# Kernel optimization log

Hardware: AMD Instinct MI355X
Metric: run time of the kernel (lower is better)

Reference implementation:

```python
import jax, jax.numpy as jnp
import numpy as np

H, KVH, HD = 32, 8, 128
DM = 4096
LN_L, LN_R = 64, 64
K_BITS, V_BITS = 4, 4
ROPE_THETA = 10000.0


def _rope(x, pos):
    # x: [B, nH, S, D], pos: [B, S]
    D = x.shape[-1]
    inv_freq = 1.0 / (ROPE_THETA ** (jnp.arange(0, D, 2, dtype=jnp.float32) / D))
    freqs = pos[:, :, None].astype(jnp.float32) * inv_freq            # [B,S,D/2]
    emb = jnp.concatenate([freqs, freqs], axis=-1)                     # [B,S,D]
    cos = jnp.cos(emb)[:, None, :, :]
    sin = jnp.sin(emb)[:, None, :, :]
    x1, x2 = x[..., : D // 2], x[..., D // 2:]
    rot = jnp.concatenate([-x2, x1], axis=-1)
    return x * cos + rot * sin


def _fake_quant(x, bits):
    # per-token (last-dim row) symmetric fake quantization
    qmax = 2.0 ** (bits - 1) - 1.0
    s = jnp.maximum(jnp.max(jnp.abs(x), axis=-1, keepdims=True) / qmax, 1e-8)
    return jnp.clip(jnp.round(x / s), -qmax, qmax) * s


def setup_inputs() -> dict:
    key = jax.random.key(0)
    ks = jax.random.split(key, 10)
    B, S = 1, 2048
    hidden_states = jax.random.normal(ks[0], (B, S, DM), dtype=jnp.float32)
    causal = jnp.tril(jnp.ones((S, S), dtype=bool))
    attention_mask = jnp.where(causal, 0.0, -1e9).astype(jnp.float32)[None, None]  # [1,1,S,S]
    position_ids = jnp.arange(S, dtype=jnp.int32)[None, :]
    sc = 1.0 / np.sqrt(DM)
    Wq = jax.random.normal(ks[1], (DM, H * HD), dtype=jnp.float32) * sc
    Wk = jax.random.normal(ks[2], (DM, KVH * HD), dtype=jnp.float32) * sc
    Wv = jax.random.normal(ks[3], (DM, KVH * HD), dtype=jnp.float32) * sc
    Wo = jax.random.normal(ks[4], (H * HD, DM), dtype=jnp.float32) * (1.0 / np.sqrt(H * HD))
    ln_left = jnp.eye(LN_L, dtype=jnp.float32) + 0.02 * jax.random.normal(ks[5], (LN_L, LN_L), dtype=jnp.float32)
    ln_right = jnp.eye(LN_R, dtype=jnp.float32) + 0.02 * jax.random.normal(ks[6], (LN_R, LN_R), dtype=jnp.float32)
    Tk = jnp.eye(HD, dtype=jnp.float32) + 0.05 * jax.random.normal(ks[7], (HD, HD), dtype=jnp.float32)
    Tv = jnp.eye(HD, dtype=jnp.float32) + 0.05 * jax.random.normal(ks[8], (HD, HD), dtype=jnp.float32)
    return {"hidden_states": hidden_states, "attention_mask": attention_mask,
            "position_ids": position_ids, "ln_left": ln_left, "ln_right": ln_right,
            "Wq": Wq, "Wk": Wk, "Wv": Wv, "Wo": Wo, "Tk": Tk, "Tv": Tv}


def reference(hidden_states, attention_mask, position_ids,
              ln_left, ln_right, Wq, Wk, Wv, Wo, Tk, Tv):
    B, S, _ = hidden_states.shape
    # ln_trans: Kronecker-decomposed SVD transform on hidden dim (64x64)
    h = hidden_states.reshape(B, S, LN_L, LN_R)
    h = jnp.einsum('bslr,la,rc->bsac', h, ln_left, ln_right).reshape(B, S, DM)
    # q/k/v projections (effective, trans-absorbed weights)
    q = (h @ Wq).reshape(B, S, H, HD).transpose(0, 2, 1, 3)    # [B,H,S,hd]
    k = (h @ Wk).reshape(B, S, KVH, HD).transpose(0, 2, 1, 3)  # [B,KVH,S,hd]
    v = ((h @ Wv).reshape(B, S, KVH, HD) @ Tv).transpose(0, 2, 1, 3)  # vcache_trans on V
    # RoPE
    q = _rope(q, position_ids)
    k = _rope(k, position_ids)
    # kcache_trans: q gets inv-transpose, k gets forward transform, then fake-quant K
    Tk_inv_t = jnp.linalg.inv(Tk).T
    q = q @ Tk_inv_t
    k = _fake_quant(k @ Tk, K_BITS)
    # vcache quant
    v = _fake_quant(v, V_BITS)
    # GQA repeat
    rep = H // KVH
    k = jnp.repeat(k, rep, axis=1)
    v = jnp.repeat(v, rep, axis=1)
    scores = jnp.einsum('bhqd,bhkd->bhqk', q, k) / np.sqrt(HD) + attention_mask
    p = jax.nn.softmax(scores.astype(jnp.float32), axis=-1).astype(q.dtype)
    o = jnp.einsum('bhqk,bhkd->bhqd', p, v).transpose(0, 2, 1, 3)  # [B,S,H,hd]
    # undo vcache_trans per head, then output projection
    o = o @ jnp.linalg.inv(Tv)
    return o.reshape(B, S, DM) @ Wo
```

## Files before the change

### kernel.cpp

```cpp
#include <hip/hip_runtime.h>
#include <math.h>

#define S_    2048
#define DM_   4096
#define H_    32
#define KVH_  8
#define HD_   128

typedef __bf16 bf16x8 __attribute__((ext_vector_type(8)));
typedef float  f32x4  __attribute__((ext_vector_type(4)));
typedef unsigned short u16x8 __attribute__((ext_vector_type(8)));
typedef unsigned short ushort_t;

__device__ __forceinline__ ushort_t f2b(float f) {
  unsigned int u = __float_as_uint(f);
  unsigned int r = (u + 0x7fffu + ((u >> 16) & 1u)) >> 16;
  return (ushort_t)r;
}
__device__ __forceinline__ float b2f(ushort_t h) {
  return __uint_as_float(((unsigned int)h) << 16);
}
__device__ __forceinline__ bf16x8 asbf(u16x8 v) {
  return __builtin_bit_cast(bf16x8, v);
}

__device__ __forceinline__ void gload16(const void* g, void* l) {
  __builtin_amdgcn_global_load_lds(
      (const __attribute__((address_space(1))) void*)g,
      (__attribute__((address_space(3))) void*)(unsigned int)(unsigned long long)l,
      16, 0, 0);
}

__global__ void newton_init(const float* __restrict__ A0, const float* __restrict__ A1,
                            float* __restrict__ X0, float* __restrict__ X1)
{
  const float* A = blockIdx.x ? A1 : A0;
  float*       X = blockIdx.x ? X1 : X0;
  const int i = blockIdx.y * 1024 + threadIdx.x;
  const int r = i >> 7, c = i & 127;
  X[i] = ((r == c) ? 2.0f : 0.0f) - A[i];
}

__global__ __launch_bounds__(256) void nmm(
    const float* __restrict__ A0, const float* __restrict__ B0, float* __restrict__ C0, int tr0,
    const float* __restrict__ A1, const float* __restrict__ B1, float* __restrict__ C1, int tr1,
    int update)
{
  const float* A = blockIdx.y ? A1 : A0;
  const float* B = blockIdx.y ? B1 : B0;
  float*       C = blockIdx.y ? C1 : C0;
  const int tr   = blockIdx.y ? tr1 : tr0;
  const int m0   = blockIdx.x * 32;
  const int tid  = threadIdx.x;

  __shared__ float Bs[128][132];
  __shared__ float As[32][132];

#pragma unroll
  for (int i = 0; i < 16; ++i) {
    int idx = tid + i * 256;
    int row = idx >> 5, c4 = (idx & 31) * 4;
    *(float4*)&Bs[row][c4] = *(const float4*)&B[row * 128 + c4];
  }
#pragma unroll
  for (int i = 0; i < 4; ++i) {
    int idx = tid + i * 256;
    int row = idx >> 5, c4 = (idx & 31) * 4;
    *(float4*)&As[row][c4] = *(const float4*)&A[(m0 + row) * 128 + c4];
  }
  __syncthreads();

  const int rloc = tid >> 3;
  const int c0   = (tid & 7) * 16;
  float acc[16];
#pragma unroll
  for (int j = 0; j < 16; ++j) acc[j] = 0.0f;
  for (int k = 0; k < 128; ++k) {
    float a = As[rloc][k];
#pragma unroll
    for (int j = 0; j < 16; j += 4) {
      float4 bv = *(const float4*)&Bs[k][c0 + j];
      acc[j + 0] += a * bv.x; acc[j + 1] += a * bv.y;
      acc[j + 2] += a * bv.z; acc[j + 3] += a * bv.w;
    }
  }
#pragma unroll
  for (int j = 0; j < 16; ++j) {
    float v = update ? (2.0f * As[rloc][c0 + j] - acc[j]) : acc[j];
    if (tr) C[(c0 + j) * 128 + (m0 + rloc)] = v;
    else    C[(m0 + rloc) * 128 + c0 + j]   = v;
  }
}

__global__ void ttrans(const float* __restrict__ in, float* __restrict__ out)
{
  __shared__ float t[32][33];
  const int bx = blockIdx.x * 32, by = blockIdx.y * 32;
  const int r = threadIdx.x >> 5, c = threadIdx.x & 31;
#pragma unroll
  for (int i = 0; i < 4; ++i)
    t[r + i * 8][c] = in[(by + r + i * 8) * 128 + bx + c];
  __syncthreads();
#pragma unroll
  for (int i = 0; i < 4; ++i)
    out[(bx + r + i * 8) * 128 + by + c] = t[c][r + i * 8];
}

__global__ void tfrag_prep(const float* __restrict__ T0, const float* __restrict__ T1,
                           const float* __restrict__ T2,
                           ushort_t* __restrict__ Fhi, ushort_t* __restrict__ Flo)
{
  const int mat = blockIdx.x;
  const float* src = (mat == 0) ? T0 : ((mat == 1) ? T1 : T2);
  ushort_t* hi = Fhi + mat * 16384;
  ushort_t* lo = Flo + mat * 16384;
  const int t = threadIdx.x;
  for (int ch = 0; ch < 32; ++ch) {
    int nt = ch >> 2, ds = ch & 3;
#pragma unroll
    for (int i = 0; i < 2; ++i) {
      int idx = t + i * 256;
      int ln = idx >> 3, j = idx & 7;
      int cc = ln & 15, gg = ln >> 4;
      int d = ds * 32 + gg * 8 + j, n = nt * 16 + cc;
      float x = src[d * 128 + n];
      ushort_t hb = f2b(x);
      hi[(ch << 9) + idx] = hb;
      lo[(ch << 9) + idx] = f2b(x - b2f(hb));
    }
  }
}

__global__ void rope_table(const int* __restrict__ pos,
                           float* __restrict__ cosT, float* __restrict__ sinT)
{
  const int s = blockIdx.x, i = threadIdx.x;
  float invf = 1.0f / (float)pow(10000.0, (double)i * (1.0 / 64.0));
  float ang  = (float)pos[s] * invf;
  cosT[s * 64 + i] = cosf(ang);
  sinT[s * 64 + i] = sinf(ang);
}

__global__ __launch_bounds__(256) void ln2(const float* __restrict__ hid,
                                           const float* __restrict__ L,
                                           const float* __restrict__ R,
                                           ushort_t* __restrict__ hb16,
                                           ushort_t* __restrict__ hlo16)
{
  __shared__ float B0[64 * 68];
  __shared__ float B1[64 * 68];
  __shared__ float B2[64 * 68];
  const int s   = blockIdx.x;
  const int tid = threadIdx.x;
  const float* hrow = hid + (size_t)s * DM_;

  for (int i = tid; i < 1024; i += 256) {
    int rr = i >> 4, q4 = (i & 15) * 4;
    *(float4*)&B0[rr * 68 + q4] = *(const float4*)&hrow[rr * 64 + q4];
    *(float4*)&B1[rr * 68 + q4] = *(const float4*)&R[rr * 64 + q4];
  }
  __syncthreads();

  const int row = tid >> 2;
  const int c0  = (tid & 3) * 16;
  float acc[16];
#pragma unroll
  for (int j = 0; j < 16; ++j) acc[j] = 0.0f;
  for (int rr = 0; rr < 64; ++rr) {
    float hv = B0[row * 68 + rr];
#pragma unroll
    for (int j = 0; j < 16; j += 4) {
      float4 rv = *(const float4*)&B1[rr * 68 + c0 + j];
      acc[j + 0] += hv * rv.x; acc[j + 1] += hv * rv.y;
      acc[j + 2] += hv * rv.z; acc[j + 3] += hv * rv.w;
    }
  }
#pragma unroll
  for (int j = 0; j < 16; j += 4)
    *(float4*)&B2[row * 68 + c0 + j] = make_float4(acc[j], acc[j+1], acc[j+2], acc[j+3]);
  __syncthreads();
  for (int i = tid; i < 1024; i += 256) {
    int rr = i >> 4, q4 = (i & 15) * 4;
    *(float4*)&B1[rr * 68 + q4] = *(const float4*)&L[rr * 64 + q4];
  }
  __syncthreads();

#pragma unroll
  for (int j = 0; j < 16; ++j) acc[j] = 0.0f;
  for (int ll = 0; ll < 64; ++ll) {
    float lv = B1[ll * 68 + row];
#pragma unroll
    for (int j = 0; j < 16; j += 4) {
      float4 tv = *(const float4*)&B2[ll * 68 + c0 + j];
      acc[j + 0] += lv * tv.x; acc[j + 1] += lv * tv.y;
      acc[j + 2] += lv * tv.z; acc[j + 3] += lv * tv.w;
    }
  }
  const size_t base = (size_t)s * DM_ + row * 64 + c0;
  u16x8 hv0, hv1, lv0, lv1;
#pragma unroll
  for (int j = 0; j < 8; ++j) {
    ushort_t h = f2b(acc[j]);     hv0[j] = h; lv0[j] = f2b(acc[j] - b2f(h));
    ushort_t g = f2b(acc[j + 8]); hv1[j] = g; lv1[j] = f2b(acc[j + 8] - b2f(g));
  }
  *(u16x8*)&hb16[base]      = hv0;
  *(u16x8*)&hb16[base + 8]  = hv1;
  *(u16x8*)&hlo16[base]     = lv0;
  *(u16x8*)&hlo16[base + 8] = lv1;
}

__global__ void wtrans(const float* __restrict__ W, ushort_t* __restrict__ WT,
                       int K, int N)
{
  __shared__ ushort_t t[64][68];
  const int tid = threadIdx.x;
  const int n0 = blockIdx.x * 64, k0 = blockIdx.y * 64;
  for (int idx = tid; idx < 4096; idx += 256) {
    int rr = idx >> 6, cc = idx & 63;
    t[cc][rr] = f2b(W[(size_t)(k0 + rr) * N + n0 + cc]);
  }
  __syncthreads();
  for (int idx = tid; idx < 4096; idx += 256) {
    int rr = idx >> 6, cc = idx & 63;
    WT[(size_t)(n0 + rr) * K + k0 + cc] = t[rr][cc];
  }
}

__global__ void wtrans_hl(const float* __restrict__ W,
                          ushort_t* __restrict__ WThi, ushort_t* __restrict__ WTlo,
                          int K, int N, int rowoff)
{
  __shared__ ushort_t th[64][68];
  __shared__ ushort_t tl[64][68];
  const int tid = threadIdx.x;
  const int n0 = blockIdx.x * 64, k0 = blockIdx.y * 64;
  for (int idx = tid; idx < 4096; idx += 256) {
    int rr = idx >> 6, cc = idx & 63;
    float x = W[(size_t)(k0 + rr) * N + n0 + cc];
    ushort_t h = f2b(x);
    th[cc][rr] = h;
    tl[cc][rr] = f2b(x - b2f(h));
  }
  __syncthreads();
  for (int idx = tid; idx < 4096; idx += 256) {
    int rr = idx >> 6, cc = idx & 63;
    size_t o = (size_t)(rowoff + n0 + rr) * K + k0 + cc;
    WThi[o] = th[rr][cc];
    WTlo[o] = tl[rr][cc];
  }
}

__global__ __launch_bounds__(256) void wfold2(const float* __restrict__ Wo,
                                              const float* __restrict__ TvIT,
                                              ushort_t* __restrict__ WT)
{
  const int n0g = blockIdx.x * 128;
  const int h   = blockIdx.y;
  const int tid = threadIdx.x;
  __shared__ float Ws[32][132];
  __shared__ float Tt[32][132];
  __shared__ __align__(16) ushort_t Ts[128][136];

  const int dg = tid >> 3, ng = tid & 7;
  const int d0 = dg * 4, n0 = ng * 16;

  float acc[4][16];
#pragma unroll
  for (int di = 0; di < 4; ++di)
#pragma unroll
    for (int nl = 0; nl < 16; ++nl) acc[di][nl] = 0.0f;

  for (int e0 = 0; e0 < 128; e0 += 32) {
    __syncthreads();
#pragma unroll
    for (int i = 0; i < 4; ++i) {
      int idx = tid + i * 256;
      int row = idx >> 5, c4 = (idx & 31) * 4;
      *(float4*)&Ws[row][c4] =
          *(const float4*)&Wo[(size_t)(h * 128 + e0 + row) * DM_ + n0g + c4];
      *(float4*)&Tt[row][c4] = *(const float4*)&TvIT[(e0 + row) * 128 + c4];
    }
    __syncthreads();
    for (int e = 0; e < 32; ++e) {
      float4 tv = *(const float4*)&Tt[e][d0];
#pragma unroll
      for (int j = 0; j < 4; ++j) {
        float4 wv = *(const float4*)&Ws[e][n0 + j * 4];
        acc[0][j*4+0] += tv.x*wv.x; acc[0][j*4+1] += tv.x*wv.y; acc[0][j*4+2] += tv.x*wv.z; acc[0][j*4+3] += tv.x*wv.w;
        acc[1][j*4+0] += tv.y*wv.x; acc[1][j*4+1] += tv.y*wv.y; acc[1][j*4+2] += tv.y*wv.z; acc[1][j*4+3] += tv.y*wv.w;
        acc[2][j*4+0] += tv.z*wv.x; acc[2][j*4+1] += tv.z*wv.y; acc[2][j*4+2] += tv.z*wv.z; acc[2][j*4+3] += tv.z*wv.w;
        acc[3][j*4+0] += tv.w*wv.x; acc[3][j*4+1] += tv.w*wv.y; acc[3][j*4+2] += tv.w*wv.z; acc[3][j*4+3] += tv.w*wv.w;
      }
    }
  }

#pragma unroll
  for (int di = 0; di < 4; ++di)
#pragma unroll
    for (int nl = 0; nl < 16; ++nl)
      Ts[n0 + nl][d0 + di] = f2b(acc[di][nl]);
  __syncthreads();
#pragma unroll
  for (int i = 0; i < 8; ++i) {
    int idx = tid + i * 256;
    int n = idx >> 4, c8 = (idx & 15) * 8;
    *(u16x8*)&WT[(size_t)(n0g + n) * DM_ + h * 128 + c8] = *(u16x8*)&Ts[n][c8];
  }
}

__global__ __launch_bounds__(256) void gemm_bf16(const ushort_t* __restrict__ A,
                                                 const ushort_t* __restrict__ BT,
                                                 float* __restrict__ C,
                                                 int M, int N, int K, int qlayout)
{
  __shared__ __align__(16) ushort_t As[128 * 64];
  __shared__ __align__(16) ushort_t Bs[128 * 64];
  const int tid = threadIdx.x;
  const int bm = blockIdx.y * 128, bn = blockIdx.x * 128;
  const int lane = tid & 63, w = tid >> 6;
  const int c = lane & 15, g = lane >> 4;
  const int wm = (w >> 1) * 64, wn = (w & 1) * 64;
  f32x4 acc[4][4];
#pragma unroll
  for (int mt = 0; mt < 4; ++mt)
#pragma unroll
    for (int nt = 0; nt < 4; ++nt) acc[mt][nt] = (f32x4){0.f, 0.f, 0.f, 0.f};
  const int srow = tid >> 3;
  const int slot = (tid & 7) ^ (srow & 7);
  for (int k0 = 0; k0 < K; k0 += 64) {
    __syncthreads();
#pragma unroll
    for (int ii = 0; ii < 4; ++ii) {
      gload16(A  + (size_t)(bm + ii * 32 + srow) * K + k0 + slot * 8,
              (char*)As + w * 1024 + ii * 4096);
      gload16(BT + (size_t)(bn + ii * 32 + srow) * K + k0 + slot * 8,
              (char*)Bs + w * 1024 + ii * 4096);
    }
    __syncthreads();
#pragma unroll
    for (int ks = 0; ks < 2; ++ks) {
      bf16x8 av[4], bv[4];
#pragma unroll
      for (int mt = 0; mt < 4; ++mt)
        av[mt] = *(const bf16x8*)((const char*)As + (wm + mt * 16 + c) * 128 +
                                  (((ks * 4 + g) ^ (c & 7)) << 4));
#pragma unroll
      for (int nt = 0; nt < 4; ++nt)
        bv[nt] = *(const bf16x8*)((const char*)Bs + (wn + nt * 16 + c) * 128 +
                                  (((ks * 4 + g) ^ (c & 7)) << 4));
#pragma unroll
      for (int mt = 0; mt < 4; ++mt)
#pragma unroll
        for (int nt = 0; nt < 4; ++nt)
          acc[mt][nt] = __builtin_amdgcn_mfma_f32_16x16x32_bf16(av[mt], bv[nt], acc[mt][nt], 0, 0, 0);
    }
  }
#pragma unroll
  for (int mt = 0; mt < 4; ++mt)
#pragma unroll
    for (int nt = 0; nt < 4; ++nt)
#pragma unroll
      for (int reg = 0; reg < 4; ++reg) {
        int m = bm + wm + mt * 16 + g * 4 + reg;
        int n = bn + wn + nt * 16 + c;
        float v = acc[mt][nt][reg];
        if (qlayout) C[((size_t)(n >> 7) * S_ + m) * 128 + (n & 127)] = v;
        else         C[(size_t)m * N + n] = v;
      }
}

__global__ __launch_bounds__(256) void gemm_bf16_3(
    const ushort_t* __restrict__ Ahi, const ushort_t* __restrict__ Alo,
    const ushort_t* __restrict__ BThi, const ushort_t* __restrict__ BTlo,
    float* __restrict__ Ck, float* __restrict__ Cv, int M, int N, int K)
{
  __shared__ __align__(16) ushort_t Ash[128 * 64];
  __shared__ __align__(16) ushort_t Asl[128 * 64];
  __shared__ __align__(16) ushort_t Bsh[64 * 64];
  __shared__ __align__(16) ushort_t Bsl[64 * 64];
  const int tid = threadIdx.x;
  const int bm = blockIdx.y * 128, bn = blockIdx.x * 64;
  const int lane = tid & 63, w = tid >> 6;
  const int c = lane & 15, g = lane >> 4;
  const int wm = w * 32;
  f32x4 acc[2][4];
#pragma unroll
  for (int mt = 0; mt < 2; ++mt)
#pragma unroll
    for (int nt = 0; nt < 4; ++nt) acc[mt][nt] = (f32x4){0.f, 0.f, 0.f, 0.f};
  const int srow = tid >> 3;
  const int slot = (tid & 7) ^ (srow & 7);
  for (int k0 = 0; k0 < K; k0 += 64) {
    __syncthreads();
#pragma unroll
    for (int ii = 0; ii < 4; ++ii) {
      const size_t ga = (size_t)(bm + ii * 32 + srow) * K + k0 + slot * 8;
      gload16(Ahi + ga, (char*)Ash + w * 1024 + ii * 4096);
      gload16(Alo + ga, (char*)Asl + w * 1024 + ii * 4096);
    }
#pragma unroll
    for (int ii = 0; ii < 2; ++ii) {
      const size_t gb = (size_t)(bn + ii * 32 + srow) * K + k0 + slot * 8;
      gload16(BThi + gb, (char*)Bsh + w * 1024 + ii * 4096);
      gload16(BTlo + gb, (char*)Bsl + w * 1024 + ii * 4096);
    }
    __syncthreads();
#pragma unroll
    for (int ks = 0; ks < 2; ++ks) {
      bf16x8 ah[2], al[2], bh[4], bl[4];
#pragma unroll
      for (int mt = 0; mt < 2; ++mt) {
        int ro = (wm + mt * 16 + c) * 128;
        int so = ((ks * 4 + g) ^ (c & 7)) << 4;
        ah[mt] = *(const bf16x8*)((const char*)Ash + ro + so);
        al[mt] = *(const bf16x8*)((const char*)Asl + ro + so);
      }
#pragma unroll
      for (int nt = 0; nt < 4; ++nt) {
        int ro = (nt * 16 + c) * 128;
        int so = ((ks * 4 + g) ^ (c & 7)) << 4;
        bh[nt] = *(const bf16x8*)((const char*)Bsh + ro + so);
        bl[nt] = *(const bf16x8*)((const char*)Bsl + ro + so);
      }
#pragma unroll
      for (int mt = 0; mt < 2; ++mt)
#pragma unroll
        for (int nt = 0; nt < 4; ++nt) {
          acc[mt][nt] = __builtin_amdgcn_mfma_f32_16x16x32_bf16(ah[mt], bh[nt], acc[mt][nt], 0, 0, 0);
          acc[mt][nt] = __builtin_amdgcn_mfma_f32_16x16x32_bf16(ah[mt], bl[nt], acc[mt][nt], 0, 0, 0);
          acc[mt][nt] = __builtin_amdgcn_mfma_f32_16x16x32_bf16(al[mt], bh[nt], acc[mt][nt], 0, 0, 0);
        }
    }
  }
#pragma unroll
  for (int mt = 0; mt < 2; ++mt)
#pragma unroll
    for (int nt = 0; nt < 4; ++nt)
#pragma unroll
      for (int reg = 0; reg < 4; ++reg) {
        int m = bm + wm + mt * 16 + g * 4 + reg;
        int n = bn + nt * 16 + c;
        float v = acc[mt][nt][reg];
        if (n < 1024) Ck[((size_t)(n >> 7) * S_ + m) * 128 + (n & 127)] = v;
        else          Cv[((size_t)((n - 1024) >> 7) * S_ + m) * 128 + (n & 127)] = v;
      }
}

__global__ __launch_bounds__(256) void tpost_mfma(
    const float* __restrict__ src,
    const ushort_t* __restrict__ Thi, const ushort_t* __restrict__ Tlo,
    const float* __restrict__ cosT, const float* __restrict__ sinT,
    ushort_t* __restrict__ outp, int mode)
{
  const int blk = blockIdx.x;
  const int tid = threadIdx.x;
  const int w = tid >> 6, lane = tid & 63;
  const int c = lane & 15, g = lane >> 4;

  __shared__ float raw_[32 * 132];
  __shared__ float rop_[32 * 132];
  __shared__ __align__(16) ushort_t vtile[32][136];

#pragma unroll
  for (int i = 0; i < 4; ++i) {
    int idx = tid + i * 256;
    int row = idx >> 5, c4 = (idx & 31) * 4;
    *(float4*)&raw_[row * 132 + c4] =
        *(const float4*)&src[(size_t)(blk * 32 + row) * 128 + c4];
  }
  __syncthreads();

  {
    const int r = tid >> 3, co = (tid & 7) * 16;
    if (mode <= 1) {
      const int s = (blk & 63) * 32 + r;
      const float* ct = cosT + (size_t)s * 64;
      const float* st = sinT + (size_t)s * 64;
#pragma unroll
      for (int j = 0; j < 16; ++j) {
        int cc = co + j, i2 = cc & 63;
        float x = raw_[r * 132 + cc];
        float other = (cc < 64) ? raw_[r * 132 + cc + 64] : raw_[r * 132 + cc - 64];
        rop_[r * 132 + cc] = (cc < 64) ? (x * ct[i2] - other * st[i2])
                                       : (x * ct[i2] + other * st[i2]);
      }
    } else {
#pragma unroll
      for (int j = 0; j < 16; ++j) {
        int cc = co + j;
        rop_[r * 132 + cc] = raw_[r * 132 + cc];
      }
    }
  }
  __syncthreads();

  u16x8 ahu[2][4], alu[2][4];
#pragma unroll
  for (int mt = 0; mt < 2; ++mt)
#pragma unroll
    for (int ds = 0; ds < 4; ++ds) {
      u16x8 th, tl;
#pragma unroll
      for (int j = 0; j < 8; ++j) {
        float x = rop_[(mt * 16 + c) * 132 + ds * 32 + g * 8 + j];
        ushort_t hb = f2b(x);
        th[j] = hb;
        tl[j] = f2b(x - b2f(hb));
      }
      ahu[mt][ds] = th;
      alu[mt][ds] = tl;
    }

  f32x4 acc[2][2];
#pragma unroll
  for (int mt = 0; mt < 2; ++mt)
#pragma unroll
    for (int nl = 0; nl < 2; ++nl) acc[mt][nl] = (f32x4){0.f, 0.f, 0.f, 0.f};
#pragma unroll
  for (int nl = 0; nl < 2; ++nl) {
    const int nt = w * 2 + nl;
    u16x8 bh[4], bl[4];
#pragma unroll
    for (int ds = 0; ds < 4; ++ds) {
      bh[ds] = *(const u16x8*)(Thi + ((nt * 4 + ds) << 9) + lane * 8);
      bl[ds] = *(const u16x8*)(Tlo + ((nt * 4 + ds) << 9) + lane * 8);
    }
#pragma unroll
    for (int mt = 0; mt < 2; ++mt)
#pragma unroll
      for (int ds = 0; ds < 4; ++ds) {
        acc[mt][nl] = __builtin_amdgcn_mfma_f32_16x16x32_bf16(asbf(ahu[mt][ds]), asbf(bh[ds]), acc[mt][nl], 0, 0, 0);
        acc[mt][nl] = __builtin_amdgcn_mfma_f32_16x16x32_bf16(asbf(ahu[mt][ds]), asbf(bl[ds]), acc[mt][nl], 0, 0, 0);
        acc[mt][nl] = __builtin_amdgcn_mfma_f32_16x16x32_bf16(asbf(alu[mt][ds]), asbf(bh[ds]), acc[mt][nl], 0, 0, 0);
      }
  }
  __syncthreads();

#pragma unroll
  for (int mt = 0; mt < 2; ++mt)
#pragma unroll
    for (int nl = 0; nl < 2; ++nl)
#pragma unroll
      for (int reg = 0; reg < 4; ++reg)
        raw_[(mt * 16 + g * 4 + reg) * 132 + (w * 2 + nl) * 16 + c] = acc[mt][nl][reg];
  __syncthreads();

  const int r = tid >> 3, co = (tid & 7) * 16;
  float vals[16];
#pragma unroll
  for (int j = 0; j < 16; ++j) vals[j] = raw_[r * 132 + co + j];

  if (mode == 0) {
#pragma unroll
    for (int j = 0; j < 16; ++j) vals[j] *= 0.08838834764831845f;
  } else {
    float m = 0.0f;
#pragma unroll
    for (int j = 0; j < 16; ++j) m = fmaxf(m, fabsf(vals[j]));
    m = fmaxf(m, __shfl_xor(m, 1));
    m = fmaxf(m, __shfl_xor(m, 2));
    m = fmaxf(m, __shfl_xor(m, 4));
    const float sc = fmaxf(m * (1.0f / 7.0f), 1e-8f);
#pragma unroll
    for (int j = 0; j < 16; ++j) {
      float qv = rintf(vals[j] / sc);
      qv = fminf(7.0f, fmaxf(-7.0f, qv));
      vals[j] = qv * sc;
    }
  }

  if (mode <= 1) {
    const size_t chunkbase = ((size_t)blk << 13) +
                             ((size_t)((r >> 4) * 4 + (co >> 5)) << 10);
    const int lane0 = ((co >> 3) & 3) * 16 + (r & 15);
    const int lane1 = (((co + 8) >> 3) & 3) * 16 + (r & 15);
    u16x8 o0, o1;
#pragma unroll
    for (int j = 0; j < 8; ++j) { o0[j] = f2b(vals[j]); o1[j] = f2b(vals[j + 8]); }
    *(u16x8*)((char*)outp + chunkbase + lane0 * 16) = o0;
    *(u16x8*)((char*)outp + chunkbase + lane1 * 16) = o1;
  } else {
#pragma unroll
    for (int j = 0; j < 16; ++j) vtile[r][co + j] = f2b(vals[j]);
    __syncthreads();
#pragma unroll
    for (int i = 0; i < 2; ++i) {
      int id = tid + i * 256;
      int dt = id >> 6, ln = id & 63;
      int gg = ln >> 4, cc = ln & 15;
      u16x8 o;
#pragma unroll
      for (int j = 0; j < 8; ++j) o[j] = vtile[gg * 8 + j][dt * 16 + cc];
      *(u16x8*)(outp + (((size_t)blk) << 12) + (dt << 9) + ln * 8) = o;
    }
  }
}

__global__ __launch_bounds__(256) void attn_mfma6(
    const ushort_t* __restrict__ qf_,
    const ushort_t* __restrict__ kf_,
    const ushort_t* __restrict__ vf_,
    ushort_t* __restrict__ o16)
{
  const int lid = blockIdx.x;
  const int xcd = lid & 7;
  const int idx = lid >> 3;
  const int h   = xcd * 4 + (idx & 3);
  const int kb  = idx >> 2;
  const int kvh = xcd;

  const int tid = threadIdx.x;
  const int w    = tid >> 6;
  const int lane = tid & 63;
  const int c = lane & 15, g = lane >> 4;
  const int qt = (w < 2) ? (2 * kb + w) : (60 - 2 * kb + w);

  __shared__ __align__(16) ushort_t Ps[4][2][16][40];

  const float LOG2E = 1.44269504f;
  const float MBIAS = 28.8539008f;

  const char* qtile = (const char*)qf_ + (((size_t)(h * 64 + qt)) << 13);
  bf16x8 qf[2][4];
#pragma unroll
  for (int mt = 0; mt < 2; ++mt)
#pragma unroll
    for (int ds = 0; ds < 4; ++ds)
      qf[mt][ds] = *(const bf16x8*)(qtile + ((mt * 4 + ds) << 10) + lane * 16);

  bf16x8 ones;
#pragma unroll
  for (int j = 0; j < 8; ++j) ones[j] = (__bf16)1.0f;

  f32x4 oa[2][8];
#pragma unroll
  for (int mt = 0; mt < 2; ++mt)
#pragma unroll
    for (int dt = 0; dt < 8; ++dt) oa[mt][dt] = (f32x4){0.f, 0.f, 0.f, 0.f};
  f32x4 la[2];
  la[0] = (f32x4){0.f, 0.f, 0.f, 0.f};
  la[1] = (f32x4){0.f, 0.f, 0.f, 0.f};

  const char* kbase = (const char*)kf_ + (((size_t)kvh * 64) << 13);
  const char* vbase = (const char*)vf_ + (((size_t)kvh * 64) << 13);

  for (int kt = 0; kt <= qt; ++kt) {
    const char* ktile = kbase + ((size_t)kt << 13);
    const char* vtile = vbase + ((size_t)kt << 13);
    bf16x8 kc[2][4], vc[8];
#pragma unroll
    for (int nt = 0; nt < 2; ++nt)
#pragma unroll
      for (int ds = 0; ds < 4; ++ds)
        kc[nt][ds] = *(const bf16x8*)(ktile + ((nt * 4 + ds) << 10) + lane * 16);
#pragma unroll
    for (int dt = 0; dt < 8; ++dt)
      vc[dt] = *(const bf16x8*)(vtile + (dt << 10) + lane * 16);

    f32x4 sc[2][2];
#pragma unroll
    for (int mt = 0; mt < 2; ++mt)
#pragma unroll
      for (int nt = 0; nt < 2; ++nt) sc[mt][nt] = (f32x4){0.f, 0.f, 0.f, 0.f};
    __builtin_amdgcn_s_setprio(1);
#pragma unroll
    for (int ds = 0; ds < 4; ++ds) {
      sc[0][0] = __builtin_amdgcn_mfma_f32_16x16x32_bf16(qf[0][ds], kc[0][ds], sc[0][0], 0, 0, 0);
      sc[0][1] = __builtin_amdgcn_mfma_f32_16x16x32_bf16(qf[0][ds], kc[1][ds], sc[0][1], 0, 0, 0);
      sc[1][0] = __builtin_amdgcn_mfma_f32_16x16x32_bf16(qf[1][ds], kc[0][ds], sc[1][0], 0, 0, 0);
      sc[1][1] = __builtin_amdgcn_mfma_f32_16x16x32_bf16(qf[1][ds], kc[1][ds], sc[1][1], 0, 0, 0);
    }
    __builtin_amdgcn_s_setprio(0);

#pragma unroll
    for (int mt = 0; mt < 2; ++mt) {
#pragma unroll
      for (int reg = 0; reg < 4; ++reg) {
        float s0 = sc[mt][0][reg], s1 = sc[mt][1][reg];
        if (kt == qt) {
          int qrl = mt * 16 + g * 4 + reg;
          if (c > qrl)      s0 = -INFINITY;
          if (16 + c > qrl) s1 = -INFINITY;
        }
        float p0 = exp2f(s0 * LOG2E - MBIAS);
        float p1 = exp2f(s1 * LOG2E - MBIAS);
        Ps[w][mt][g * 4 + reg][c]      = f2b(p0);
        Ps[w][mt][g * 4 + reg][16 + c] = f2b(p1);
      }
    }

    bf16x8 pa0 = *reinterpret_cast<const bf16x8*>(&Ps[w][0][c][g * 8]);
    bf16x8 pa1 = *reinterpret_cast<const bf16x8*>(&Ps[w][1][c][g * 8]);
    __builtin_amdgcn_s_setprio(1);
#pragma unroll
    for (int dt = 0; dt < 8; ++dt) {
      oa[0][dt] = __builtin_amdgcn_mfma_f32_16x16x32_bf16(pa0, vc[dt], oa[0][dt], 0, 0, 0);
      oa[1][dt] = __builtin_amdgcn_mfma_f32_16x16x32_bf16(pa1, vc[dt], oa[1][dt], 0, 0, 0);
    }
    la[0] = __builtin_amdgcn_mfma_f32_16x16x32_bf16(pa0, ones, la[0], 0, 0, 0);
    la[1] = __builtin_amdgcn_mfma_f32_16x16x32_bf16(pa1, ones, la[1], 0, 0, 0);
    __builtin_amdgcn_s_setprio(0);
  }

#pragma unroll
  for (int mt = 0; mt < 2; ++mt)
#pragma unroll
    for (int reg = 0; reg < 4; ++reg) {
      float li = 1.0f / la[mt][reg];
      int srow = qt * 32 + mt * 16 + g * 4 + reg;
      ushort_t* orow = o16 + (size_t)srow * DM_ + h * 128;
#pragma unroll
      for (int dt = 0; dt < 8; ++dt)
        orow[dt * 16 + c] = f2b(oa[mt][dt][reg] * li);
    }
}

extern "C" void kernel_launch(void* const* d_in, const int* in_sizes, int n_in,
                              void* d_out, int out_size, void* d_ws, size_t ws_size,
                              hipStream_t stream)
{
  (void)in_sizes; (void)n_in; (void)out_size; (void)ws_size;
  const float* hidden = (const float*)d_in[0];
  const int*   pos    = (const int*)d_in[2];
  const float* lnL    = (const float*)d_in[3];
  const float* lnR    = (const float*)d_in[4];
  const float* Wq     = (const float*)d_in[5];
  const float* Wk     = (const float*)d_in[6];
  const float* Wv     = (const float*)d_in[7];
  const float* Wo     = (const float*)d_in[8];
  const float* Tk     = (const float*)d_in[9];
  const float* Tv     = (const float*)d_in[10];
  float* out = (float*)d_out;

  float* ws   = (float*)d_ws;
  float* hbuf = ws;
  float* kbuf = hbuf + (size_t)S_ * DM_;
  float* vbuf = kbuf + (size_t)S_ * KVH_ * HD_;
  float* Tkit = vbuf + (size_t)S_ * KVH_ * HD_;
  float* TvI  = Tkit + 128 * 128;
  float* cosT = TvI + 128 * 128;
  float* sinT = cosT + (size_t)S_ * 64;
  ushort_t* hb16 = (ushort_t*)(sinT + (size_t)S_ * 64);
  ushort_t* WT   = hb16 + (size_t)S_ * DM_;
  float* nb      = (float*)(WT + (size_t)DM_ * DM_);
  float* TvIT    = nb + 6 * 16384;
  ushort_t* tfH  = (ushort_t*)(TvIT + 16384);
  ushort_t* tfL  = tfH + 3 * 16384;

  char* hbytes = (char*)hbuf;
  ushort_t* hlo16 = (ushort_t*)hbytes;
  ushort_t* qfrag = (ushort_t*)hbytes;
  ushort_t* kfrag = (ushort_t*)(hbytes + (16u << 20));
  ushort_t* vfrag = (ushort_t*)(hbytes + (20u << 20));

  ushort_t* WTkh = WT;
  ushort_t* WTkl = WT + (size_t)2048 * DM_;

  float* Xk = nb,              *Xv = nb + 16384;
  float* Yk = nb + 2 * 16384,  *Yv = nb + 3 * 16384;
  float* Xk2 = nb + 4 * 16384, *Xv2 = nb + 5 * 16384;

  float* qbuf = out;

  newton_init<<<dim3(2, 16), 1024, 0, stream>>>(Tk, Tv, Xk, Xv);
  for (int it = 0; it < 4; ++it) {
    nmm<<<dim3(4, 2), 256, 0, stream>>>(Tk, Xk, Yk, 0, Tv, Xv, Yv, 0, 0);
    const int last = (it == 3);
    float* ok = last ? Tkit : Xk2;
    float* ov = last ? TvI  : Xv2;
    nmm<<<dim3(4, 2), 256, 0, stream>>>(Xk, Yk, ok, last ? 1 : 0, Xv, Yv, ov, 0, 1);
    float* t;
    t = Xk; Xk = Xk2; Xk2 = t;
    t = Xv; Xv = Xv2; Xv2 = t;
  }
  ttrans<<<dim3(4, 4), 256, 0, stream>>>(TvI, TvIT);
  tfrag_prep<<<3, 256, 0, stream>>>(Tkit, Tk, Tv, tfH, tfL);

  rope_table<<<S_, 64, 0, stream>>>(pos, cosT, sinT);
  ln2<<<S_, 256, 0, stream>>>(hidden, lnL, lnR, hb16, hlo16);

  wtrans<<<dim3(DM_ / 64, DM_ / 64), 256, 0, stream>>>(Wq, WT, DM_, DM_);
  gemm_bf16<<<dim3(DM_ / 128, S_ / 128), 256, 0, stream>>>(hb16, WT, qbuf, S_, DM_, DM_, 1);
  wtrans_hl<<<dim3(16, 64), 256, 0, stream>>>(Wk, WTkh, WTkl, DM_, 1024, 0);
  wtrans_hl<<<dim3(16, 64), 256, 0, stream>>>(Wv, WTkh, WTkl, DM_, 1024, 1024);
  gemm_bf16_3<<<dim3(32, S_ / 128), 256, 0, stream>>>(hb16, hlo16, WTkh, WTkl,
                                                      kbuf, vbuf, S_, 2048, DM_);

  tpost_mfma<<<H_ * S_ / 32, 256, 0, stream>>>(qbuf, tfH,             tfL,
                                               cosT, sinT, qfrag, 0);
  tpost_mfma<<<KVH_ * S_ / 32, 256, 0, stream>>>(kbuf, tfH + 16384,   tfL + 16384,
                                                 cosT, sinT, kfrag, 1);
  tpost_mfma<<<KVH_ * S_ / 32, 256, 0, stream>>>(vbuf, tfH + 2 * 16384, tfL + 2 * 16384,
                                                 cosT, sinT, vfrag, 2);

  attn_mfma6<<<dim3(S_ / 128 * H_), 256, 0, stream>>>(qfrag, kfrag, vfrag, hb16);

  wfold2<<<dim3(DM_ / 128, H_), 256, 0, stream>>>(Wo, TvIT, WT);
  gemm_bf16<<<dim3(DM_ / 128, S_ / 128), 256, 0, stream>>>(hb16, WT, out, S_, DM_, DM_, 0);
}
```

Measured before the change: 640.7 us.

## Move LN Kronecker transform and Wo fold onto split-bf16 MFMA

Replaces the scalar FP32 ln2 kernel with ln3, which handles four tokens per block. ln3 does both 64x64 matmuls with bf16 hi/lo split MFMA (three products each), using operands prepacked by a new pack64 kernel. The scalar wfold2 Wo·Tv⁻¹ fold becomes wfold3, built the same way on MFMA, with TvIT fragments added to tfrag_prep. This trades FP32 FMA work for matrix-core throughput and keeps near-FP32 accuracy through the hi/lo split. ln3 contains an odd redundant store loop that writes hb16 twice.

```diff
diff --git a/kernel.cpp b/kernel.cpp
--- a/kernel.cpp
+++ b/kernel.cpp
@@ -107,11 +107,11 @@
 }
 
 __global__ void tfrag_prep(const float* __restrict__ T0, const float* __restrict__ T1,
-                           const float* __restrict__ T2,
+                           const float* __restrict__ T2, const float* __restrict__ T3,
                            ushort_t* __restrict__ Fhi, ushort_t* __restrict__ Flo)
 {
   const int mat = blockIdx.x;
-  const float* src = (mat == 0) ? T0 : ((mat == 1) ? T1 : T2);
+  const float* src = (mat == 0) ? T0 : ((mat == 1) ? T1 : ((mat == 2) ? T2 : T3));
   ushort_t* hi = Fhi + mat * 16384;
   ushort_t* lo = Flo + mat * 16384;
   const int t = threadIdx.x;
@@ -131,6 +131,29 @@
   }
 }
 
+__global__ void pack64(const float* __restrict__ R, const float* __restrict__ L,
+                       ushort_t* __restrict__ RBh, ushort_t* __restrict__ RBl,
+                       ushort_t* __restrict__ LBh, ushort_t* __restrict__ LBl)
+{
+  const float* src = blockIdx.x ? L : R;
+  ushort_t* hp = blockIdx.x ? LBh : RBh;
+  ushort_t* lp = blockIdx.x ? LBl : RBl;
+  const int t = threadIdx.x;
+  for (int ch = 0; ch < 8; ++ch) {
+    int nt = ch >> 1, ds = ch & 1;
+#pragma unroll
+    for (int i = 0; i < 2; ++i) {
+      int idx = t + i * 256;
+      int ln = idx >> 3, j = idx & 7;
+      int cc = ln & 15, gg = ln >> 4;
+      float x = src[(ds * 32 + gg * 8 + j) * 64 + nt * 16 + cc];
+      ushort_t hb = f2b(x);
+      hp[(ch << 9) + idx] = hb;
+      lp[(ch << 9) + idx] = f2b(x - b2f(hb));
+    }
+  }
+}
+
 __global__ void rope_table(const int* __restrict__ pos,
                            float* __restrict__ cosT, float* __restrict__ sinT)
 {
@@ -141,72 +164,136 @@
   sinT[s * 64 + i] = sinf(ang);
 }
 
-__global__ __launch_bounds__(256) void ln2(const float* __restrict__ hid,
-                                           const float* __restrict__ L,
-                                           const float* __restrict__ R,
-                                           ushort_t* __restrict__ hb16,
-                                           ushort_t* __restrict__ hlo16)
-{
-  __shared__ float B0[64 * 68];
-  __shared__ float B1[64 * 68];
-  __shared__ float B2[64 * 68];
-  const int s   = blockIdx.x;
+__global__ __launch_bounds__(256) void ln3(
+    const float* __restrict__ hid,
+    const ushort_t* __restrict__ RBh, const ushort_t* __restrict__ RBl,
+    const ushort_t* __restrict__ LBh, const ushort_t* __restrict__ LBl,
+    ushort_t* __restrict__ hb16, ushort_t* __restrict__ hlo16)
+{
+  const int blk = blockIdx.x;
   const int tid = threadIdx.x;
-  const float* hrow = hid + (size_t)s * DM_;
-
-  for (int i = tid; i < 1024; i += 256) {
-    int rr = i >> 4, q4 = (i & 15) * 4;
-    *(float4*)&B0[rr * 68 + q4] = *(const float4*)&hrow[rr * 64 + q4];
-    *(float4*)&B1[rr * 68 + q4] = *(const float4*)&R[rr * 64 + q4];
-  }
-  __syncthreads();
-
-  const int row = tid >> 2;
-  const int c0  = (tid & 3) * 16;
-  float acc[16];
-#pragma unroll
-  for (int j = 0; j < 16; ++j) acc[j] = 0.0f;
-  for (int rr = 0; rr < 64; ++rr) {
-    float hv = B0[row * 68 + rr];
-#pragma unroll
-    for (int j = 0; j < 16; j += 4) {
-      float4 rv = *(const float4*)&B1[rr * 68 + c0 + j];
-      acc[j + 0] += hv * rv.x; acc[j + 1] += hv * rv.y;
-      acc[j + 2] += hv * rv.z; acc[j + 3] += hv * rv.w;
-    }
-  }
-#pragma unroll
-  for (int j = 0; j < 16; j += 4)
-    *(float4*)&B2[row * 68 + c0 + j] = make_float4(acc[j], acc[j+1], acc[j+2], acc[j+3]);
-  __syncthreads();
-  for (int i = tid; i < 1024; i += 256) {
-    int rr = i >> 4, q4 = (i & 15) * 4;
-    *(float4*)&B1[rr * 68 + q4] = *(const float4*)&L[rr * 64 + q4];
-  }
-  __syncthreads();
-
-#pragma unroll
-  for (int j = 0; j < 16; ++j) acc[j] = 0.0f;
-  for (int ll = 0; ll < 64; ++ll) {
-    float lv = B1[ll * 68 + row];
-#pragma unroll
-    for (int j = 0; j < 16; j += 4) {
-      float4 tv = *(const float4*)&B2[ll * 68 + c0 + j];
-      acc[j + 0] += lv * tv.x; acc[j + 1] += lv * tv.y;
-      acc[j + 2] += lv * tv.z; acc[j + 3] += lv * tv.w;
-    }
-  }
-  const size_t base = (size_t)s * DM_ + row * 64 + c0;
-  u16x8 hv0, hv1, lv0, lv1;
-#pragma unroll
-  for (int j = 0; j < 8; ++j) {
-    ushort_t h = f2b(acc[j]);     hv0[j] = h; lv0[j] = f2b(acc[j] - b2f(h));
-    ushort_t g = f2b(acc[j + 8]); hv1[j] = g; lv1[j] = f2b(acc[j + 8] - b2f(g));
-  }
-  *(u16x8*)&hb16[base]      = hv0;
-  *(u16x8*)&hb16[base + 8]  = hv1;
-  *(u16x8*)&hlo16[base]     = lv0;
-  *(u16x8*)&hlo16[base + 8] = lv1;
+  const int w = tid >> 6, lane = tid & 63;
+  const int c = lane & 15, g = lane >> 4;
+
+  __shared__ float Hs[4][64 * 68];
+
+#pragma unroll
+  for (int i = 0; i < 16; ++i) {
+    int idx = tid + i * 256;
+    int t = idx >> 10, e = idx & 1023;
+    int l = e >> 4, r4 = (e & 15) * 4;
+    *(float4*)&Hs[t][l * 68 + r4] =
+        *(const float4*)&hid[((size_t)(blk * 4 + t)) * 4096 + l * 64 + r4];
+  }
+  __syncthreads();
+
+  float* Hw = Hs[w];
+
+  u16x8 ah[4][2], al[4][2];
+#pragma unroll
+  for (int mt = 0; mt < 4; ++mt)
+#pragma unroll
+    for (int ds = 0; ds < 2; ++ds) {
+      u16x8 th, tl;
+#pragma unroll
+      for (int j = 0; j < 8; ++j) {
+        float x = Hw[(mt * 16 + c) * 68 + ds * 32 + g * 8 + j];
+        ushort_t hb = f2b(x); th[j] = hb; tl[j] = f2b(x - b2f(hb));
+      }
+      ah[mt][ds] = th; al[mt][ds] = tl;
+    }
+
+  f32x4 acc[4][4];
+#pragma unroll
+  for (int mt = 0; mt < 4; ++mt)
+#pragma unroll
+    for (int nt = 0; nt < 4; ++nt) acc[mt][nt] = (f32x4){0.f, 0.f, 0.f, 0.f};
+#pragma unroll
+  for (int nt = 0; nt < 4; ++nt) {
+    u16x8 bh[2], bl[2];
+#pragma unroll
+    for (int ds = 0; ds < 2; ++ds) {
+      bh[ds] = *(const u16x8*)(RBh + ((nt * 2 + ds) << 9) + lane * 8);
+      bl[ds] = *(const u16x8*)(RBl + ((nt * 2 + ds) << 9) + lane * 8);
+    }
+#pragma unroll
+    for (int mt = 0; mt < 4; ++mt)
+#pragma unroll
+      for (int ds = 0; ds < 2; ++ds) {
+        acc[mt][nt] = __builtin_amdgcn_mfma_f32_16x16x32_bf16(asbf(ah[mt][ds]), asbf(bh[ds]), acc[mt][nt], 0, 0, 0);
+        acc[mt][nt] = __builtin_amdgcn_mfma_f32_16x16x32_bf16(asbf(ah[mt][ds]), asbf(bl[ds]), acc[mt][nt], 0, 0, 0);
+        acc[mt][nt] = __builtin_amdgcn_mfma_f32_16x16x32_bf16(asbf(al[mt][ds]), asbf(bh[ds]), acc[mt][nt], 0, 0, 0);
+      }
+  }
+
+#pragma unroll
+  for (int mt = 0; mt < 4; ++mt)
+#pragma unroll
+    for (int nt = 0; nt < 4; ++nt)
+#pragma unroll
+      for (int reg = 0; reg < 4; ++reg)
+        Hw[(mt * 16 + g * 4 + reg) * 68 + nt * 16 + c] = acc[mt][nt][reg];
+
+  u16x8 a2h[4][2], a2l[4][2];
+#pragma unroll
+  for (int mt = 0; mt < 4; ++mt)
+#pragma unroll
+    for (int ds = 0; ds < 2; ++ds) {
+      a2h[mt][ds] = *(const u16x8*)(LBh + ((mt * 2 + ds) << 9) + lane * 8);
+      a2l[mt][ds] = *(const u16x8*)(LBl + ((mt * 2 + ds) << 9) + lane * 8);
+    }
+  f32x4 acc2[4][4];
+#pragma unroll
+  for (int mt = 0; mt < 4; ++mt)
+#pragma unroll
+    for (int nt = 0; nt < 4; ++nt) acc2[mt][nt] = (f32x4){0.f, 0.f, 0.f, 0.f};
+#pragma unroll
+  for (int nt = 0; nt < 4; ++nt) {
+#pragma unroll
+    for (int ds = 0; ds < 2; ++ds) {
+      u16x8 bh, bl;
+#pragma unroll
+      for (int j = 0; j < 8; ++j) {
+        float x = Hw[(ds * 32 + g * 8 + j) * 68 + nt * 16 + c];
+        ushort_t hb = f2b(x); bh[j] = hb; bl[j] = f2b(x - b2f(hb));
+      }
+#pragma unroll
+      for (int mt = 0; mt < 4; ++mt) {
+        acc2[mt][nt] = __builtin_amdgcn_mfma_f32_16x16x32_bf16(asbf(a2h[mt][ds]), asbf(bh), acc2[mt][nt], 0, 0, 0);
+        acc2[mt][nt] = __builtin_amdgcn_mfma_f32_16x16x32_bf16(asbf(a2h[mt][ds]), asbf(bl), acc2[mt][nt], 0, 0, 0);
+        acc2[mt][nt] = __builtin_amdgcn_mfma_f32_16x16x32_bf16(asbf(a2l[mt][ds]), asbf(bh), acc2[mt][nt], 0, 0, 0);
+      }
+    }
+  }
+
+  ushort_t* hp = (ushort_t*)Hw;
+#pragma unroll
+  for (int mt = 0; mt < 4; ++mt)
+#pragma unroll
+    for (int nt = 0; nt < 4; ++nt)
+#pragma unroll
+      for (int reg = 0; reg < 4; ++reg) {
+        int a = mt * 16 + g * 4 + reg, cc2 = nt * 16 + c;
+        float v = acc2[mt][nt][reg];
+        ushort_t hb = f2b(v);
+        hp[a * 64 + cc2] = hb;
+        hp[4096 + a * 64 + cc2] = f2b(v - b2f(hb));
+      }
+
+  const size_t sbase = ((size_t)(blk * 4 + w)) * 4096;
+#pragma unroll
+  for (int i = 0; i < 8; ++i) {
+    int idx = i * 64 + lane;
+    int row = idx >> 3, c8 = (idx & 7) * 8;
+    *(u16x8*)&hb16[sbase + row * 64 * 8 / 8 * 1 + row * 0 + row * 64 + c8 - row * 64] = *(const u16x8*)&hp[row * 64 + c8];
+  }
+#pragma unroll
+  for (int i = 0; i < 8; ++i) {
+    int idx = i * 64 + lane;
+    int row = idx >> 3, c8 = (idx & 7) * 8;
+    *(u16x8*)&hb16[sbase + row * 64 + c8]  = *(const u16x8*)&hp[row * 64 + c8];
+    *(u16x8*)&hlo16[sbase + row * 64 + c8] = *(const u16x8*)&hp[4096 + row * 64 + c8];
+  }
 }
 
 __global__ void wtrans(const float* __restrict__ W, ushort_t* __restrict__ WT,
@@ -250,61 +337,78 @@
   }
 }
 
-__global__ __launch_bounds__(256) void wfold2(const float* __restrict__ Wo,
-                                              const float* __restrict__ TvIT,
-                                              ushort_t* __restrict__ WT)
-{
-  const int n0g = blockIdx.x * 128;
-  const int h   = blockIdx.y;
+__global__ __launch_bounds__(256) void wfold3(
+    const float* __restrict__ Wo,
+    const ushort_t* __restrict__ TBh, const ushort_t* __restrict__ TBl,
+    ushort_t* __restrict__ WT)
+{
+  const int n0 = blockIdx.x * 128;
+  const int h  = blockIdx.y;
   const int tid = threadIdx.x;
-  __shared__ float Ws[32][132];
-  __shared__ float Tt[32][132];
-  __shared__ __align__(16) ushort_t Ts[128][136];
-
-  const int dg = tid >> 3, ng = tid & 7;
-  const int d0 = dg * 4, n0 = ng * 16;
-
-  float acc[4][16];
-#pragma unroll
-  for (int di = 0; di < 4; ++di)
-#pragma unroll
-    for (int nl = 0; nl < 16; ++nl) acc[di][nl] = 0.0f;
-
-  for (int e0 = 0; e0 < 128; e0 += 32) {
-    __syncthreads();
-#pragma unroll
-    for (int i = 0; i < 4; ++i) {
-      int idx = tid + i * 256;
-      int row = idx >> 5, c4 = (idx & 31) * 4;
-      *(float4*)&Ws[row][c4] =
-          *(const float4*)&Wo[(size_t)(h * 128 + e0 + row) * DM_ + n0g + c4];
-      *(float4*)&Tt[row][c4] = *(const float4*)&TvIT[(e0 + row) * 128 + c4];
-    }
-    __syncthreads();
-    for (int e = 0; e < 32; ++e) {
-      float4 tv = *(const float4*)&Tt[e][d0];
-#pragma unroll
-      for (int j = 0; j < 4; ++j) {
-        float4 wv = *(const float4*)&Ws[e][n0 + j * 4];
-        acc[0][j*4+0] += tv.x*wv.x; acc[0][j*4+1] += tv.x*wv.y; acc[0][j*4+2] += tv.x*wv.z; acc[0][j*4+3] += tv.x*wv.w;
-        acc[1][j*4+0] += tv.y*wv.x; acc[1][j*4+1] += tv.y*wv.y; acc[1][j*4+2] += tv.y*wv.z; acc[1][j*4+3] += tv.y*wv.w;
-        acc[2][j*4+0] += tv.z*wv.x; acc[2][j*4+1] += tv.z*wv.y; acc[2][j*4+2] += tv.z*wv.z; acc[2][j*4+3] += tv.z*wv.w;
-        acc[3][j*4+0] += tv.w*wv.x; acc[3][j*4+1] += tv.w*wv.y; acc[3][j*4+2] += tv.w*wv.z; acc[3][j*4+3] += tv.w*wv.w;
-      }
-    }
-  }
-
-#pragma unroll
-  for (int di = 0; di < 4; ++di)
-#pragma unroll
-    for (int nl = 0; nl < 16; ++nl)
-      Ts[n0 + nl][d0 + di] = f2b(acc[di][nl]);
-  __syncthreads();
+  const int w = tid >> 6, lane = tid & 63;
+  const int c = lane & 15, g = lane >> 4;
+
+  __shared__ float WoS[128 * 132];
+
+#pragma unroll
+  for (int i = 0; i < 16; ++i) {
+    int idx = tid + i * 256;
+    int e = idx >> 5, n4 = (idx & 31) * 4;
+    *(float4*)&WoS[e * 132 + n4] =
+        *(const float4*)&Wo[(size_t)(h * 128 + e) * 4096 + n0 + n4];
+  }
+  __syncthreads();
+
+  u16x8 ah[2][4], al[2][4];
+#pragma unroll
+  for (int mt = 0; mt < 2; ++mt)
+#pragma unroll
+    for (int ds = 0; ds < 4; ++ds) {
+      u16x8 th, tl;
+#pragma unroll
+      for (int j = 0; j < 8; ++j) {
+        float x = WoS[(ds * 32 + g * 8 + j) * 132 + w * 32 + mt * 16 + c];
+        ushort_t hb = f2b(x); th[j] = hb; tl[j] = f2b(x - b2f(hb));
+      }
+      ah[mt][ds] = th; al[mt][ds] = tl;
+    }
+
+  f32x4 acc[2][8];
+#pragma unroll
+  for (int mt = 0; mt < 2; ++mt)
+#pragma unroll
+    for (int nt = 0; nt < 8; ++nt) acc[mt][nt] = (f32x4){0.f, 0.f, 0.f, 0.f};
+#pragma unroll
+  for (int nt = 0; nt < 8; ++nt) {
+#pragma unroll
+    for (int ds = 0; ds < 4; ++ds) {
+      u16x8 bh = *(const u16x8*)(TBh + ((nt * 4 + ds) << 9) + lane * 8);
+      u16x8 bl = *(const u16x8*)(TBl + ((nt * 4 + ds) << 9) + lane * 8);
+#pragma unroll
+      for (int mt = 0; mt < 2; ++mt) {
+        acc[mt][nt] = __builtin_amdgcn_mfma_f32_16x16x32_bf16(asbf(ah[mt][ds]), asbf(bh), acc[mt][nt], 0, 0, 0);
+        acc[mt][nt] = __builtin_amdgcn_mfma_f32_16x16x32_bf16(asbf(ah[mt][ds]), asbf(bl), acc[mt][nt], 0, 0, 0);
+        acc[mt][nt] = __builtin_amdgcn_mfma_f32_16x16x32_bf16(asbf(al[mt][ds]), asbf(bh), acc[mt][nt], 0, 0, 0);
+      }
+    }
+  }
+  __syncthreads();
+
+  ushort_t* OS = (ushort_t*)WoS;
+#pragma unroll
+  for (int mt = 0; mt < 2; ++mt)
+#pragma unroll
+    for (int nt = 0; nt < 8; ++nt)
+#pragma unroll
+      for (int reg = 0; reg < 4; ++reg)
+        OS[(w * 32 + mt * 16 + g * 4 + reg) * 136 + nt * 16 + c] = f2b(acc[mt][nt][reg]);
+  __syncthreads();
+
 #pragma unroll
   for (int i = 0; i < 8; ++i) {
     int idx = tid + i * 256;
-    int n = idx >> 4, c8 = (idx & 15) * 8;
-    *(u16x8*)&WT[(size_t)(n0g + n) * DM_ + h * 128 + c8] = *(u16x8*)&Ts[n][c8];
+    int nn = idx >> 4, c8 = (idx & 15) * 8;
+    *(u16x8*)&WT[(size_t)(n0 + nn) * 4096 + h * 128 + c8] = *(const u16x8*)&OS[nn * 136 + c8];
   }
 }
 
@@ -745,7 +849,11 @@
   float* nb      = (float*)(WT + (size_t)DM_ * DM_);
   float* TvIT    = nb + 6 * 16384;
   ushort_t* tfH  = (ushort_t*)(TvIT + 16384);
-  ushort_t* tfL  = tfH + 3 * 16384;
+  ushort_t* tfL  = tfH + 4 * 16384;
+  ushort_t* RBh  = tfL + 4 * 16384;
+  ushort_t* RBl  = RBh + 4096;
+  ushort_t* LBh  = RBl + 4096;
+  ushort_t* LBl  = LBh + 4096;
 
   char* hbytes = (char*)hbuf;
   ushort_t* hlo16 = (ushort_t*)hbytes;
@@ -774,10 +882,11 @@
     t = Xv; Xv = Xv2; Xv2 = t;
   }
   ttrans<<<dim3(4, 4), 256, 0, stream>>>(TvI, TvIT);
-  tfrag_prep<<<3, 256, 0, stream>>>(Tkit, Tk, Tv, tfH, tfL);
+  tfrag_prep<<<4, 256, 0, stream>>>(Tkit, Tk, Tv, TvIT, tfH, tfL);
+  pack64<<<2, 256, 0, stream>>>(lnR, lnL, RBh, RBl, LBh, LBl);
 
   rope_table<<<S_, 64, 0, stream>>>(pos, cosT, sinT);
-  ln2<<<S_, 256, 0, stream>>>(hidden, lnL, lnR, hb16, hlo16);
+  ln3<<<S_ / 4, 256, 0, stream>>>(hidden, RBh, RBl, LBh, LBl, hb16, hlo16);
 
   wtrans<<<dim3(DM_ / 64, DM_ / 64), 256, 0, stream>>>(Wq, WT, DM_, DM_);
   gemm_bf16<<<dim3(DM_ / 128, S_ / 128), 256, 0, stream>>>(hb16, WT, qbuf, S_, DM_, DM_, 1);
@@ -795,6 +904,6 @@
 
   attn_mfma6<<<dim3(S_ / 128 * H_), 256, 0, stream>>>(qfrag, kfrag, vfrag, hb16);
 
-  wfold2<<<dim3(DM_ / 128, H_), 256, 0, stream>>>(Wo, TvIT, WT);
+  wfold3<<<dim3(DM_ / 128, H_), 256, 0, stream>>>(Wo, tfH + 3 * 16384, tfL + 3 * 16384, WT);
   gemm_bf16<<<dim3(DM_ / 128, S_ / 128), 256, 0, stream>>>(hb16, WT, out, S_, DM_, DM_, 0);
 }
```

Result: faster. 587.2 us (-8.4%).
